# Performance work log

Measured on AMD Instinct MI355X. Metric: run time of the kernel, lower is better.

The kernel has to match this reference:

```python
import jax, jax.numpy as jnp
import numpy as np

EPS = 1e-5
H = 8  # attention heads


def _bn(f, g, b):
    # MinkowskiBatchNorm: per-channel batch-norm over all N points (training stats)
    mu = f.mean(0)
    var = f.var(0)
    return g * (f - mu) * jax.lax.rsqrt(var + EPS) + b


def setup_inputs() -> dict:
    key = jax.random.key(0)
    ks = jax.random.split(key, 8)
    B, GS, ED = 8, 1024, 512
    N = B * GS
    s = 1.0 / np.sqrt(ED)
    inp = {
        "x": jax.random.normal(ks[0], (N, ED), jnp.float32),
        "mask": jnp.ones((B, GS), bool),
        "Wq": jax.random.normal(ks[1], (ED, ED), jnp.float32) * s,
        "bq": jnp.zeros((ED,), jnp.float32),
        "Wk": jax.random.normal(ks[2], (ED, ED), jnp.float32) * s,
        "bk": jnp.zeros((ED,), jnp.float32),
        "Wv": jax.random.normal(ks[3], (ED, ED), jnp.float32) * s,
        "bv": jnp.zeros((ED,), jnp.float32),
        "Wo": jax.random.normal(ks[4], (ED, ED), jnp.float32) * s,
        "bo": jnp.zeros((ED,), jnp.float32),
        "g1": jnp.ones((ED,), jnp.float32),
        "be1": jnp.zeros((ED,), jnp.float32),
        "g2": jnp.ones((ED,), jnp.float32),
        "be2": jnp.zeros((ED,), jnp.float32),
        "W1": jax.random.normal(ks[5], (ED, 4 * ED), jnp.float32) * s,
        "b1m": jnp.zeros((4 * ED,), jnp.float32),
        "W2": jax.random.normal(ks[6], (4 * ED, ED), jnp.float32) * (0.5 * s),
        "b2m": jnp.zeros((ED,), jnp.float32),
        "b": B,
        "gs": GS,
    }
    return inp


def reference(x, mask, Wq, bq, Wk, bk, Wv, bv, Wo, bo, g1, be1, g2, be2, W1, b1m, W2, b2m, b, gs):
    ed = x.shape[-1]
    dh = ed // H
    # --- pre-norm + multi-head self-attention over [b, gs] groups ---
    h1 = _bn(x, g1, be1)
    q = (h1 @ Wq + bq).reshape(b, gs, H, dh)
    k = (h1 @ Wk + bk).reshape(b, gs, H, dh)
    v = (h1 @ Wv + bv).reshape(b, gs, H, dh)
    scores = jnp.einsum('bqhd,bkhd->bhqk', q, k) / jnp.sqrt(jnp.float32(dh))
    scores = jnp.where(mask[:, None, None, :], scores, jnp.float32(-1e9))
    a = jax.nn.softmax(scores, axis=-1)
    o = jnp.einsum('bhqk,bkhd->bqhd', a, v).reshape(b * gs, ed)
    x = x + (o @ Wo + bo)  # residual (dropout identity at eval/d_rate=0)
    # --- pre-norm + MLP (GELU exact, as torch default) ---
    h2 = _bn(x, g2, be2)
    m = jax.nn.gelu(h2 @ W1 + b1m, approximate=False) @ W2 + b2m
    return x + m
```

## Files before the change

kernel.cpp:

```cpp
#include <hip/hip_runtime.h>
#include <hip/hip_bf16.h>


typedef unsigned short u16;
typedef unsigned int   u32;
typedef __attribute__((ext_vector_type(8))) short bf16x8;
typedef __attribute__((ext_vector_type(4))) float f32x4;
typedef __attribute__((ext_vector_type(4))) u16   u16x4;

#define ED   512
#define NTOK 8192
#define GSZ  1024
#define NH   8
#define DH   64

__device__ __forceinline__ u16 f2bf(float f) {
    __hip_bfloat16 h = __float2bfloat16(f);
    union { __hip_bfloat16 h; u16 u; } v; v.h = h;
    return v.u;
}

__device__ __forceinline__ void gload_lds16(const u16* g, u16* lds) {
    __builtin_amdgcn_global_load_lds(
        (const __attribute__((address_space(1))) u32*)g,
        (__attribute__((address_space(3))) u32*)lds, 16, 0, 0);
}

__device__ __forceinline__ f32x4 mfma16(bf16x8 a, bf16x8 b, f32x4 c) {
    return __builtin_amdgcn_mfma_f32_16x16x32_bf16(a, b, c, 0, 0, 0);
}

__device__ __forceinline__ void xcd_swizzle(int& bx, int& by) {
    int ny = gridDim.y;
    int nwg = gridDim.x * ny;
    int wg = blockIdx.y * gridDim.x + blockIdx.x;
    int per = nwg >> 3;
    int swz = (wg & 7) * per + (wg >> 3);
    by = swz % ny;
    bx = swz / ny;
}

__global__ __launch_bounds__(256) void wt_cast(const float* __restrict__ W,
                                               u16* __restrict__ Wt, int K, int N)
{
    __shared__ float t[32][33];
    int n0 = blockIdx.x * 32, k0 = blockIdx.y * 32;
    int tx = threadIdx.x & 31, ty = threadIdx.x >> 5;
#pragma unroll
    for (int r = 0; r < 4; ++r)
        t[ty * 4 + r][tx] = W[(size_t)(k0 + ty * 4 + r) * N + n0 + tx];
    __syncthreads();
#pragma unroll
    for (int r = 0; r < 4; ++r)
        Wt[(size_t)(n0 + ty * 4 + r) * K + k0 + tx] = f2bf(t[tx][ty * 4 + r]);
}

__global__ __launch_bounds__(256) void wt_cast4(
    const float* w0, const float* w1, const float* w2, const float* w3,
    u16* o0, u16* o1, u16* o2, u16* o3)
{
    const float* W = blockIdx.z == 0 ? w0 : blockIdx.z == 1 ? w1 : blockIdx.z == 2 ? w2 : w3;
    u16*        Wt = blockIdx.z == 0 ? o0 : blockIdx.z == 1 ? o1 : blockIdx.z == 2 ? o2 : o3;
    __shared__ float t[32][33];
    int n0 = blockIdx.x * 32, k0 = blockIdx.y * 32;
    int tx = threadIdx.x & 31, ty = threadIdx.x >> 5;
#pragma unroll
    for (int r = 0; r < 4; ++r)
        t[ty * 4 + r][tx] = W[(size_t)(k0 + ty * 4 + r) * ED + n0 + tx];
    __syncthreads();
#pragma unroll
    for (int r = 0; r < 4; ++r)
        Wt[(size_t)(n0 + ty * 4 + r) * ED + k0 + tx] = f2bf(t[tx][ty * 4 + r]);
}

__global__ __launch_bounds__(512) void bn_stats(const float* __restrict__ x,
                                                float* __restrict__ psum,
                                                float* __restrict__ psq)
{
    int c = threadIdx.x, blk = blockIdx.x;
    const float* p = x + (size_t)blk * 64 * ED + c;
    float s = 0.f, q = 0.f;
#pragma unroll 4
    for (int r = 0; r < 64; ++r) { float v = p[(size_t)r * ED]; s += v; q += v * v; }
    psum[blk * ED + c] = s;
    psq [blk * ED + c] = q;
}

__global__ __launch_bounds__(512) void bn_final(const float* __restrict__ psum,
                                                const float* __restrict__ psq,
                                                const float* __restrict__ g,
                                                const float* __restrict__ be,
                                                float* __restrict__ sb)
{
    int c = threadIdx.x;
    float s = 0.f, q = 0.f;
    for (int i = 0; i < 128; ++i) { s += psum[i * ED + c]; q += psq[i * ED + c]; }
    float mu  = s * (1.f / NTOK);
    float var = q * (1.f / NTOK) - mu * mu;
    float sc  = g[c] * rsqrtf(var + 1e-5f);
    sb[c]      = sc;
    sb[ED + c] = be[c] - mu * sc;
}

__global__ __launch_bounds__(256) void bn_apply(const float* __restrict__ x,
                                                const float* __restrict__ sb,
                                                u16* __restrict__ h)
{
    size_t idx = (size_t)blockIdx.x * 256 + threadIdx.x;
    const float4 v = ((const float4*)x)[idx];
    int c = (int)((idx * 4) & (ED - 1));
    u16x4 o;
    o[0] = f2bf(v.x * sb[c + 0] + sb[ED + c + 0]);
    o[1] = f2bf(v.y * sb[c + 1] + sb[ED + c + 1]);
    o[2] = f2bf(v.z * sb[c + 2] + sb[ED + c + 2]);
    o[3] = f2bf(v.w * sb[c + 3] + sb[ED + c + 3]);
    ((u16x4*)h)[idx] = o;
}

template <int BN, int BK>
__device__ __forceinline__ void gemm_core(const u16* __restrict__ A,
                                          const u16* __restrict__ Bt,
                                          int lda, int ldb, int K,
                                          size_t arow0, size_t brow0,
                                          u16 (&As)[2][128 * BK], u16 (&Bs)[2][BN * BK],
                                          f32x4 (&acc)[4][BN / 32])
{
    constexpr int NJ   = BN / 32;
    constexpr int KH   = BK / 32;
    constexpr int SEGS = BK / 8;
    constexpr int ACH  = (128 * BK) / 2048;
    constexpr int BCH  = (BN * BK) / 2048;
    const int tid  = threadIdx.x;
    const int lane = tid & 63, wid = tid >> 6;
    const int wm = wid >> 1, wn = wid & 1;
    const int frow = lane & 15, g = lane >> 4;
#pragma unroll
    for (int i = 0; i < 4; ++i)
#pragma unroll
        for (int j = 0; j < NJ; ++j) acc[i][j] = f32x4{0.f, 0.f, 0.f, 0.f};

#define SWZSEG(SG, R) ((BK == 64) ? ((SG) ^ ((R) & 7)) : ((SG) ^ (((R) >> 1) & 3)))
#define STAGE(K0, BUF) do {                                                     \
        _Pragma("unroll")                                                       \
        for (int a_ = 0; a_ < ACH; ++a_) {                                      \
            int c_ = tid + a_ * 256; int r_ = c_ / SEGS; int sg_ = c_ % SEGS;   \
            gload_lds16(A + (arow0 + r_) * lda + (K0) + SWZSEG(sg_, r_) * 8,    \
                        &As[BUF][c_ * 8]);                                      \
        }                                                                       \
        _Pragma("unroll")                                                       \
        for (int b_ = 0; b_ < BCH; ++b_) {                                      \
            int c_ = tid + b_ * 256; int r_ = c_ / SEGS; int sg_ = c_ % SEGS;   \
            gload_lds16(Bt + (brow0 + r_) * ldb + (K0) + SWZSEG(sg_, r_) * 8,   \
                        &Bs[BUF][c_ * 8]);                                      \
        }                                                                       \
    } while (0)

    STAGE(0, 0);
    __syncthreads();

    const int nt = K / BK;
    for (int t = 0; t < nt; ++t) {
        const int cur = t & 1;
        if (t + 1 < nt) STAGE((t + 1) * BK, cur ^ 1);
        const char* Ac = (const char*)&As[cur][0];
        const char* Bc = (const char*)&Bs[cur][0];
        bf16x8 af[4][KH], bfr[NJ][KH];
#pragma unroll
        for (int i = 0; i < 4; ++i) {
            int row = wm * 64 + i * 16 + frow;
#pragma unroll
            for (int kh = 0; kh < KH; ++kh) {
                int byte = row * (2 * BK) + kh * 64 + g * 16;
                byte ^= (BK == 64) ? ((row & 7) << 4) : ((row & 6) << 3);
                af[i][kh] = *(const bf16x8*)(Ac + byte);
            }
        }
#pragma unroll
        for (int j = 0; j < NJ; ++j) {
            int row = wn * (BN / 2) + j * 16 + frow;
#pragma unroll
            for (int kh = 0; kh < KH; ++kh) {
                int byte = row * (2 * BK) + kh * 64 + g * 16;
                byte ^= (BK == 64) ? ((row & 7) << 4) : ((row & 6) << 3);
                bfr[j][kh] = *(const bf16x8*)(Bc + byte);
            }
        }
#pragma unroll
        for (int kh = 0; kh < KH; ++kh)
#pragma unroll
            for (int i = 0; i < 4; ++i)
#pragma unroll
                for (int j = 0; j < NJ; ++j)
                    acc[i][j] = mfma16(af[i][kh], bfr[j][kh], acc[i][j]);
        __syncthreads();
    }
#undef STAGE
#undef SWZSEG
}

__global__ __launch_bounds__(256) void qkv_gemm(
    const u16* __restrict__ h1,
    const u16* __restrict__ wqT, const u16* __restrict__ wkT, const u16* __restrict__ wvT,
    const float* __restrict__ bq, const float* __restrict__ bk, const float* __restrict__ bv,
    u16* __restrict__ Q, u16* __restrict__ Kb, u16* __restrict__ Vt)
{
    __shared__ u16 As[2][4096];
    __shared__ u16 Bs[2][4096];
    int bx, by;
    xcd_swizzle(bx, by);
    int mb = bx;
    int which = by >> 2;
    int nloc = (by & 3) * 128;
    const u16*  Bt   = which == 0 ? wqT : (which == 1 ? wkT : wvT);
    const float* bias = which == 0 ? bq : (which == 1 ? bk : bv);
    f32x4 acc[4][4];
    gemm_core<128, 32>(h1, Bt, ED, ED, ED, (size_t)mb * 128, (size_t)nloc, As, Bs, acc);

    int lane = threadIdx.x & 63, wid = threadIdx.x >> 6;
    int wm = wid >> 1, wn = wid & 1, G = lane >> 4, r16 = lane & 15;
    int colb = nloc + wn * 64 + r16;
    float bsc[4];
#pragma unroll
    for (int j = 0; j < 4; ++j) bsc[j] = bias[colb + j * 16];

    if (which == 2) {
#pragma unroll
        for (int i = 0; i < 4; ++i) {
            int row0 = mb * 128 + wm * 64 + i * 16 + G * 4;
            int bidx = row0 >> 10, kv = row0 & (GSZ - 1);
#pragma unroll
            for (int j = 0; j < 4; ++j) {
                int col = colb + j * 16;
                int hh = col >> 6, d = col & 63;
                u16x4 pk;
#pragma unroll
                for (int r = 0; r < 4; ++r) pk[r] = f2bf(acc[i][j][r] + bsc[j]);
                *(u16x4*)(Vt + ((size_t)((bidx * NH + hh) * DH + d)) * GSZ + kv) = pk;
            }
        }
    } else {
        float scale = which == 0 ? 0.18033688011112042f : 1.0f;
        u16* Dst = which == 0 ? Q : Kb;
#pragma unroll
        for (int i = 0; i < 4; ++i) {
            int row = mb * 128 + wm * 64 + i * 16 + G * 4;
#pragma unroll
            for (int j = 0; j < 4; ++j) {
                int col = colb + j * 16;
#pragma unroll
                for (int r = 0; r < 4; ++r)
                    Dst[(size_t)(row + r) * ED + col] = f2bf((acc[i][j][r] + bsc[j]) * scale);
            }
        }
    }
}

template <int MODE, int BN, int BK>
__global__ __launch_bounds__(256) void gemm_epi(
    const u16* __restrict__ A, const u16* __restrict__ Bt, const float* __restrict__ bias,
    const float* res, float* outf, u16* outb, int K, int N)
{
    __shared__ u16 As[2][128 * BK];
    __shared__ u16 Bs[2][BN * BK];
    constexpr int NJ = BN / 32;
    int bx, by;
    xcd_swizzle(bx, by);
    f32x4 acc[4][NJ];
    gemm_core<BN, BK>(A, Bt, K, K, K, (size_t)bx * 128, (size_t)by * BN, As, Bs, acc);

    int lane = threadIdx.x & 63, wid = threadIdx.x >> 6;
    int wm = wid >> 1, wn = wid & 1, G = lane >> 4, r16 = lane & 15;
    int colb = by * BN + wn * (BN / 2) + r16;
    float bsc[NJ];
#pragma unroll
    for (int j = 0; j < NJ; ++j) bsc[j] = bias[colb + j * 16];
#pragma unroll
    for (int i = 0; i < 4; ++i) {
        int row = bx * 128 + wm * 64 + i * 16 + G * 4;
#pragma unroll
        for (int j = 0; j < NJ; ++j) {
            int col = colb + j * 16;
#pragma unroll
            for (int r = 0; r < 4; ++r) {
                float v = acc[i][j][r] + bsc[j];
                size_t o = (size_t)(row + r) * N + col;
                if (MODE == 1) {
                    outf[o] = v + res[o];
                } else {
                    float gl = 0.5f * v * (1.f + erff(v * 0.70710678118654752f));
                    outb[o] = f2bf(gl);
                }
            }
        }
    }
}

__global__ __launch_bounds__(512) void attn(const u16* __restrict__ Q,
                                            const u16* __restrict__ Kb,
                                            const u16* __restrict__ Vt,
                                            u16* __restrict__ O)
{
    __shared__ u16 KS[2][4096];
    __shared__ u16 VS[2][4096];
    __shared__ u16 P[8][1024];

    const int qt = blockIdx.x, bh = blockIdx.y;
    const int b = bh >> 3, h = bh & 7;
    const int tid = threadIdx.x, lane = tid & 63, w = tid >> 6;
    const int G = lane >> 4, r16 = lane & 15;
    char* Pw = (char*)&P[w][0];
    const int qbase = qt * 128 + w * 16;
    const int swz = (r16 & 7) << 4;

    const u16* kbase = Kb + ((size_t)b * GSZ) * ED + h * DH;
    const u16* vbase = Vt + ((size_t)bh * DH) * GSZ;

    const int c0 = tid;
    const int row0 = c0 >> 3, seg0 = (c0 & 7) ^ (row0 & 7);

    bf16x8 aq[2];
#pragma unroll
    for (int ks = 0; ks < 2; ++ks)
        aq[ks] = *(const bf16x8*)(Q + (size_t)(b * GSZ + qbase + r16) * ED
                                  + h * DH + ks * 32 + G * 8);

    bf16x8 ones;
#pragma unroll
    for (int i = 0; i < 8; ++i) ones[i] = (short)0x3F80;

    f32x4 o[4];
#pragma unroll
    for (int dt = 0; dt < 4; ++dt) o[dt] = f32x4{0.f, 0.f, 0.f, 0.f};
    f32x4 o_l = f32x4{0.f, 0.f, 0.f, 0.f};
    float m = -3e38f;

    gload_lds16(kbase + (size_t)row0 * ED + seg0 * 8, &KS[0][0] + c0 * 8);
    gload_lds16(vbase + (size_t)row0 * GSZ + seg0 * 8, &VS[0][0] + c0 * 8);
    __syncthreads();

    for (int c = 0; c < 16; ++c) {
        const int cur = c & 1;
        if (c < 15) {
            int kv0 = (c + 1) * 64;
            gload_lds16(kbase + (size_t)(kv0 + row0) * ED + seg0 * 8, &KS[cur ^ 1][0] + c0 * 8);
            gload_lds16(vbase + (size_t)row0 * GSZ + kv0 + seg0 * 8, &VS[cur ^ 1][0] + c0 * 8);
        }
        const char* Kc = (const char*)&KS[cur][0];
        const char* Vc = (const char*)&VS[cur][0];

        f32x4 s[4];
#pragma unroll
        for (int t = 0; t < 4; ++t) s[t] = f32x4{0.f, 0.f, 0.f, 0.f};
#pragma unroll
        for (int t = 0; t < 4; ++t) {
            int kvrow = (t * 16 + r16) * 128;
#pragma unroll
            for (int ks = 0; ks < 2; ++ks) {
                bf16x8 bk = *(const bf16x8*)(Kc + ((kvrow + ks * 64 + G * 16) ^ swz));
                s[t] = mfma16(bk, aq[ks], s[t]);
            }
        }

        float cm = fmaxf(fmaxf(fmaxf(s[0][0], s[0][1]), fmaxf(s[0][2], s[0][3])),
                         fmaxf(fmaxf(s[1][0], s[1][1]), fmaxf(s[1][2], s[1][3])));
        float cm2 = fmaxf(fmaxf(fmaxf(s[2][0], s[2][1]), fmaxf(s[2][2], s[2][3])),
                          fmaxf(fmaxf(s[3][0], s[3][1]), fmaxf(s[3][2], s[3][3])));
        cm = fmaxf(cm, cm2);
        if (__any(cm - m > 8.f)) {
            float mx = fmaxf(cm, __shfl_xor(cm, 16, 64));
            mx = fmaxf(mx, __shfl_xor(mx, 32, 64));
            float mn = fmaxf(m, mx);
            float r = exp2f(m - mn);
            m = mn;
            float rb[4];
#pragma unroll
            for (int j = 0; j < 4; ++j) rb[j] = __shfl(r, G * 4 + j, 64);
#pragma unroll
            for (int dt = 0; dt < 4; ++dt) {
                o[dt][0] *= rb[0]; o[dt][1] *= rb[1];
                o[dt][2] *= rb[2]; o[dt][3] *= rb[3];
            }
            o_l[0] *= rb[0]; o_l[1] *= rb[1];
            o_l[2] *= rb[2]; o_l[3] *= rb[3];
        }

#pragma unroll
        for (int t = 0; t < 4; ++t) {
            u16x4 pk;
            pk[0] = f2bf(exp2f(s[t][0] - m));
            pk[1] = f2bf(exp2f(s[t][1] - m));
            pk[2] = f2bf(exp2f(s[t][2] - m));
            pk[3] = f2bf(exp2f(s[t][3] - m));
            *(u16x4*)(Pw + ((r16 * 128 + t * 32 + G * 8) ^ swz)) = pk;
        }

#pragma unroll
        for (int ks = 0; ks < 2; ++ks) {
            bf16x8 pa = *(const bf16x8*)(Pw + ((r16 * 128 + ks * 64 + G * 16) ^ swz));
            o_l = mfma16(pa, ones, o_l);
#pragma unroll
            for (int dt = 0; dt < 4; ++dt) {
                bf16x8 bv = *(const bf16x8*)(Vc + (((dt * 16 + r16) * 128 + ks * 64 + G * 16) ^ swz));
                o[dt] = mfma16(pa, bv, o[dt]);
            }
        }
        __syncthreads();
    }

    float linv[4];
#pragma unroll
    for (int j = 0; j < 4; ++j) linv[j] = 1.f / o_l[j];
#pragma unroll
    for (int dt = 0; dt < 4; ++dt)
#pragma unroll
        for (int j = 0; j < 4; ++j) {
            int row = b * GSZ + qbase + G * 4 + j;
            O[(size_t)row * ED + h * DH + dt * 16 + r16] = f2bf(o[dt][j] * linv[j]);
        }
}

extern "C" void kernel_launch(void* const* d_in, const int* in_sizes, int n_in,
                              void* d_out, int out_size, void* d_ws, size_t ws_size,
                              hipStream_t stream)
{
    const float* x   = (const float*)d_in[0];
    const float* Wq  = (const float*)d_in[2];
    const float* bq  = (const float*)d_in[3];
    const float* Wk  = (const float*)d_in[4];
    const float* bk  = (const float*)d_in[5];
    const float* Wv  = (const float*)d_in[6];
    const float* bv  = (const float*)d_in[7];
    const float* Wo  = (const float*)d_in[8];
    const float* bo  = (const float*)d_in[9];
    const float* g1  = (const float*)d_in[10];
    const float* be1 = (const float*)d_in[11];
    const float* g2  = (const float*)d_in[12];
    const float* be2 = (const float*)d_in[13];
    const float* W1  = (const float*)d_in[14];
    const float* b1m = (const float*)d_in[15];
    const float* W2  = (const float*)d_in[16];
    const float* b2m = (const float*)d_in[17];
    float* out = (float*)d_out;
    char* ws = (char*)d_ws;

    u16*   wqT  = (u16*)(ws + 0);
    u16*   wkT  = (u16*)(ws + 524288);
    u16*   wvT  = (u16*)(ws + 1048576);
    u16*   woT  = (u16*)(ws + 1572864);
    u16*   w1T  = (u16*)(ws + 2097152);
    u16*   w2T  = (u16*)(ws + 4194304);
    float* sb1  = (float*)(ws + 6291456);
    float* sb2  = (float*)(ws + 6295552);
    float* psum = (float*)(ws + 6299648);
    float* psq  = (float*)(ws + 6561792);
    u16*   h1   = (u16*)(ws + 7340032);
    u16*   Qb   = (u16*)(ws + 16777216);
    u16*   Kbf  = (u16*)(ws + 25165824);
    u16*   Vt   = (u16*)(ws + 33554432);
    u16*   mid  = (u16*)(ws + 16777216);
    u16*   Ob   = h1;
    u16*   h2   = h1;

    wt_cast4<<<dim3(16, 16, 4), 256, 0, stream>>>(Wq, Wk, Wv, Wo, wqT, wkT, wvT, woT);
    wt_cast<<<dim3(64, 16), 256, 0, stream>>>(W1, w1T, ED, 4 * ED);
    wt_cast<<<dim3(16, 64), 256, 0, stream>>>(W2, w2T, 4 * ED, ED);

    bn_stats<<<128, 512, 0, stream>>>(x, psum, psq);
    bn_final<<<1, 512, 0, stream>>>(psum, psq, g1, be1, sb1);
    bn_apply<<<4096, 256, 0, stream>>>(x, sb1, h1);

    qkv_gemm<<<dim3(64, 12), 256, 0, stream>>>(h1, wqT, wkT, wvT, bq, bk, bv, Qb, Kbf, Vt);

    attn<<<dim3(8, 64), 512, 0, stream>>>(Qb, Kbf, Vt, Ob);

    gemm_epi<1, 64, 64><<<dim3(64, 8), 256, 0, stream>>>(Ob, woT, bo, x, out, nullptr, ED, ED);

    bn_stats<<<128, 512, 0, stream>>>(out, psum, psq);
    bn_final<<<1, 512, 0, stream>>>(psum, psq, g2, be2, sb2);
    bn_apply<<<4096, 256, 0, stream>>>(out, sb2, h2);

    gemm_epi<2, 128, 32><<<dim3(64, 16), 256, 0, stream>>>(h2, w1T, b1m, nullptr, nullptr, mid, ED, 4 * ED);

    gemm_epi<1, 64, 64><<<dim3(64, 8), 256, 0, stream>>>(mid, w2T, b2m, out, out, nullptr, 4 * ED, ED);
}
```

Measured before the change: 201.7 us.

## Add 256x256-tile GEMM kernel with 512 threads for the MLP up-projection

```diff
diff --git a/kernel.cpp b/kernel.cpp
--- a/kernel.cpp
+++ b/kernel.cpp
@@ -279,6 +279,102 @@
         int row = bx * 128 + wm * 64 + i * 16 + G * 4;
 #pragma unroll
         for (int j = 0; j < NJ; ++j) {
+            int col = colb + j * 16;
+#pragma unroll
+            for (int r = 0; r < 4; ++r) {
+                float v = acc[i][j][r] + bsc[j];
+                size_t o = (size_t)(row + r) * N + col;
+                if (MODE == 1) {
+                    outf[o] = v + res[o];
+                } else {
+                    float gl = 0.5f * v * (1.f + erff(v * 0.70710678118654752f));
+                    outb[o] = f2bf(gl);
+                }
+            }
+        }
+    }
+}
+
+template <int MODE>
+__global__ __launch_bounds__(512, 1) void gemm256(
+    const u16* __restrict__ A, const u16* __restrict__ Bt, const float* __restrict__ bias,
+    const float* res, float* outf, u16* outb, int K, int N)
+{
+    __shared__ u16 As[2][256 * 64];
+    __shared__ u16 Bs[2][256 * 64];
+    int bx, by;
+    xcd_swizzle(bx, by);
+    const int tid = threadIdx.x;
+    const int lane = tid & 63, wid = tid >> 6;
+    const int wm = wid >> 2, wn = wid & 3;
+    const int frow = lane & 15, g = lane >> 4;
+    const size_t arow0 = (size_t)bx * 256, brow0 = (size_t)by * 256;
+
+    f32x4 acc[8][4];
+#pragma unroll
+    for (int i = 0; i < 8; ++i)
+#pragma unroll
+        for (int j = 0; j < 4; ++j) acc[i][j] = f32x4{0.f, 0.f, 0.f, 0.f};
+
+#define STAGE256(K0, BUF) do {                                                  \
+        _Pragma("unroll")                                                       \
+        for (int a_ = 0; a_ < 4; ++a_) {                                        \
+            int c_ = tid + a_ * 512; int r_ = c_ >> 3;                          \
+            int sg_ = (c_ & 7) ^ (r_ & 7);                                      \
+            gload_lds16(A + (arow0 + r_) * K + (K0) + sg_ * 8,                  \
+                        &As[BUF][c_ * 8]);                                      \
+        }                                                                       \
+        _Pragma("unroll")                                                       \
+        for (int b_ = 0; b_ < 4; ++b_) {                                        \
+            int c_ = tid + b_ * 512; int r_ = c_ >> 3;                          \
+            int sg_ = (c_ & 7) ^ (r_ & 7);                                      \
+            gload_lds16(Bt + (brow0 + r_) * K + (K0) + sg_ * 8,                 \
+                        &Bs[BUF][c_ * 8]);                                      \
+        }                                                                       \
+    } while (0)
+
+    STAGE256(0, 0);
+    __syncthreads();
+
+    const int nt = K >> 6;
+    for (int t = 0; t < nt; ++t) {
+        const int cur = t & 1;
+        if (t + 1 < nt) STAGE256((t + 1) << 6, cur ^ 1);
+        const char* Ac = (const char*)&As[cur][0];
+        const char* Bc = (const char*)&Bs[cur][0];
+#pragma unroll
+        for (int kh = 0; kh < 2; ++kh) {
+            bf16x8 bfr[4];
+#pragma unroll
+            for (int j = 0; j < 4; ++j) {
+                int row = wn * 64 + j * 16 + frow;
+                int byte = (row * 128 + kh * 64 + g * 16) ^ ((row & 7) << 4);
+                bfr[j] = *(const bf16x8*)(Bc + byte);
+            }
+#pragma unroll
+            for (int i = 0; i < 8; ++i) {
+                int row = wm * 128 + i * 16 + frow;
+                int byte = (row * 128 + kh * 64 + g * 16) ^ ((row & 7) << 4);
+                bf16x8 af = *(const bf16x8*)(Ac + byte);
+#pragma unroll
+                for (int j = 0; j < 4; ++j)
+                    acc[i][j] = mfma16(af, bfr[j], acc[i][j]);
+            }
+        }
+        __syncthreads();
+    }
+#undef STAGE256
+
+    const int G = lane >> 4, r16 = lane & 15;
+    int colb = by * 256 + wn * 64 + r16;
+    float bsc[4];
+#pragma unroll
+    for (int j = 0; j < 4; ++j) bsc[j] = bias[colb + j * 16];
+#pragma unroll
+    for (int i = 0; i < 8; ++i) {
+        int row = bx * 256 + wm * 128 + i * 16 + G * 4;
+#pragma unroll
+        for (int j = 0; j < 4; ++j) {
             int col = colb + j * 16;
 #pragma unroll
             for (int r = 0; r < 4; ++r) {
@@ -479,7 +575,7 @@
     bn_final<<<1, 512, 0, stream>>>(psum, psq, g2, be2, sb2);
     bn_apply<<<4096, 256, 0, stream>>>(out, sb2, h2);
 
-    gemm_epi<2, 128, 32><<<dim3(64, 16), 256, 0, stream>>>(h2, w1T, b1m, nullptr, nullptr, mid, ED, 4 * ED);
+    gemm256<2><<<dim3(32, 8), 512, 0, stream>>>(h2, w1T, b1m, nullptr, nullptr, mid, ED, 4 * ED);
 
     gemm_epi<1, 64, 64><<<dim3(64, 8), 256, 0, stream>>>(mid, w2T, b2m, out, out, nullptr, 4 * ED, ED);
 }
```

New measurement: 198.3 us. About the same (-1.7%).
